# Kernel tuning notes

Hardware: AMD Instinct MI355X
Metric: run time of the kernel (lower is better)

The kernel has to match this reference:

```python
import jax, jax.numpy as jnp
import numpy as np

H = 4  # attention heads
NEG = -1e9

def _ln(x, g, b):
    m = jnp.mean(x, -1, keepdims=True)
    v = jnp.var(x, -1, keepdims=True)
    return g * (x - m) * jax.lax.rsqrt(v + 1e-5) + b

def setup_inputs() -> dict:
    key = jax.random.key(0)
    ks = jax.random.split(key, 32)
    N, E, G, T = 4096, 128, 10, 10
    f32 = jnp.float32
    def w(k, shape, fan):
        return (jax.random.normal(k, shape, f32) / np.sqrt(fan)).astype(f32)
    inp = {
        'lora_states': jax.random.normal(ks[0], (N, 256), f32),
        'temperaments': jax.random.uniform(ks[1], (N, T), f32),
        'adjacency': jax.random.randint(ks[2], (N, N), 0, 2, jnp.int32),
        'memory_bank': jax.random.normal(ks[3], (G, E), f32) * 0.1,
        # lora_state_encoder: Linear(256,512) -> LN -> ReLU -> Linear(512,E) -> LN
        'enc_W1': w(ks[4], (256, 512), 256), 'enc_b1': jnp.zeros((512,), f32),
        'enc_g1': jnp.ones((512,), f32), 'enc_be1': jnp.zeros((512,), f32),
        'enc_W2': w(ks[5], (512, E), 512), 'enc_b2': jnp.zeros((E,), f32),
        'enc_g2': jnp.ones((E,), f32), 'enc_be2': jnp.zeros((E,), f32),
        # TemperamentEncoder: Linear(10,E) + tanh
        'temp_W': w(ks[6], (T, E), T), 'temp_b': jnp.zeros((E,), f32),
        # SocialAttentionLayer (adjacency-masked MHA)
        'Wq': w(ks[7], (E, E), E), 'Wk': w(ks[8], (E, E), E),
        'Wv': w(ks[9], (E, E), E), 'Wo': w(ks[10], (E, E), E),
        # PersonalityModulatedAttention scalar gate over [my_temp; ctx_j]
        'gate_wa': w(ks[11], (E,), E), 'gate_wb': w(ks[12], (E,), E),
        'gate_b': jnp.zeros((), f32),
        # lora_state_decoder: Linear(E,512) -> LN -> ReLU -> Linear(512,256)
        'dec_W1': w(ks[13], (E, 512), E), 'dec_b1': jnp.zeros((512,), f32),
        'dec_g1': jnp.ones((512,), f32), 'dec_be1': jnp.zeros((512,), f32),
        'dec_W2': w(ks[14], (512, 256), 512), 'dec_b2': jnp.zeros((256,), f32),
    }
    return inp

def reference(lora_states, temperaments, adjacency, memory_bank,
              enc_W1, enc_b1, enc_g1, enc_be1, enc_W2, enc_b2, enc_g2, enc_be2,
              temp_W, temp_b, Wq, Wk, Wv, Wo, gate_wa, gate_wb, gate_b,
              dec_W1, dec_b1, dec_g1, dec_be1, dec_W2, dec_b2):
    N = lora_states.shape[0]
    E = Wq.shape[0]
    dh = E // H
    # --- encode LoRA states ---
    h = jax.nn.relu(_ln(lora_states @ enc_W1 + enc_b1, enc_g1, enc_be1))
    emb = _ln(h @ enc_W2 + enc_b2, enc_g2, enc_be2)                  # [N,E]
    # --- temperament embeddings ---
    temp_emb = jnp.tanh(temperaments @ temp_W + temp_b)              # [N,E]
    # --- adjacency-masked multi-head social attention ---
    q = (emb @ Wq).reshape(N, H, dh).transpose(1, 0, 2)              # [H,N,dh]
    k = (emb @ Wk).reshape(N, H, dh).transpose(1, 0, 2)
    v = (emb @ Wv).reshape(N, H, dh).transpose(1, 0, 2)
    scores = jnp.einsum('hnd,hmd->hnm', q, k) / np.sqrt(dh)          # [H,N,N]
    adj = adjacency > 0
    eye = jnp.eye(N, dtype=bool)
    attn = jax.nn.softmax(jnp.where((adj | eye)[None], scores, NEG), axis=-1)
    ctx = jnp.einsum('hnm,hmd->hnd', attn, v).transpose(1, 0, 2).reshape(N, E) @ Wo  # [N,E]
    # --- personality-gated neighbor aggregation (scalar gate per (i,j)) ---
    ti = temp_emb @ gate_wa                                          # [N]
    cj = ctx @ gate_wb                                               # [N]
    gate = jax.nn.sigmoid(ti[:, None] + cj[None, :] + gate_b)        # [N,N]
    nmask = (adj & ~eye).astype(emb.dtype)                           # exclude self
    cnt = nmask.sum(-1)                                              # [N]
    combined = (nmask * gate) @ ctx / jnp.maximum(cnt, 1.0)[:, None] # mean of gated neighbor infos
    updated = emb + 0.2 * jnp.where(cnt[:, None] > 0, combined, 0.0)
    # --- generational memory retrieval: 0.9*emb + 0.1*ancestral ---
    mscore = updated @ memory_bank.T / np.sqrt(E)                    # [N,G]
    ancestral = jax.nn.softmax(mscore, axis=-1) @ memory_bank        # [N,E]
    updated = 0.9 * updated + 0.1 * ancestral
    # --- decode back to LoRA state vectors ---
    d = jax.nn.relu(_ln(updated @ dec_W1 + dec_b1, dec_g1, dec_be1))
    return d @ dec_W2 + dec_b2                                       # [N,256]
```

## Files before the change

### kernel.cpp

```cpp
#include <hip/hip_runtime.h>
#include <math.h>

#define N 4096
#define NHEAD 4
#define SPLIT_ATT 8
#define SPLIT_G 8

__global__ __launch_bounds__(512) void k_enc1(const float* __restrict__ X,
    const float* __restrict__ W, const float* __restrict__ b,
    const float* __restrict__ g, const float* __restrict__ be,
    float* __restrict__ out) {
  __shared__ float xs[8][256];
  __shared__ float hs[8][512];
  const int t = threadIdx.x;
  const int row0 = blockIdx.x * 8;
  {
    const float4* src = reinterpret_cast<const float4*>(X + row0 * 256);
    float4* dst = reinterpret_cast<float4*>(&xs[0][0]);
    dst[t] = src[t];
  }
  __syncthreads();
  float acc[8] = {0.f,0.f,0.f,0.f,0.f,0.f,0.f,0.f};
  for (int k = 0; k < 256; ++k) {
    float w = W[k * 512 + t];
#pragma unroll
    for (int r = 0; r < 8; ++r) acc[r] = fmaf(xs[r][k], w, acc[r]);
  }
  const float bb = b[t];
#pragma unroll
  for (int r = 0; r < 8; ++r) hs[r][t] = acc[r] + bb;
  __syncthreads();
  const int wv = t >> 6, lane = t & 63;
  float v0[8];
  float s1 = 0.f, s2 = 0.f;
#pragma unroll
  for (int kk = 0; kk < 8; ++kk) {
    float x = hs[wv][lane + 64 * kk];
    v0[kk] = x; s1 += x; s2 += x * x;
  }
#pragma unroll
  for (int off = 1; off < 64; off <<= 1) { s1 += __shfl_xor(s1, off); s2 += __shfl_xor(s2, off); }
  const float mean = s1 * (1.f / 512.f);
  const float var = s2 * (1.f / 512.f) - mean * mean;
  const float rstd = rsqrtf(var + 1e-5f);
#pragma unroll
  for (int kk = 0; kk < 8; ++kk) {
    int c = lane + 64 * kk;
    float y = g[c] * (v0[kk] - mean) * rstd + be[c];
    out[(row0 + wv) * 512 + c] = fmaxf(y, 0.f);
  }
}

__global__ __launch_bounds__(128) void k_enc2(const float* __restrict__ X,
    const float* __restrict__ W, const float* __restrict__ b,
    const float* __restrict__ g, const float* __restrict__ be,
    float* __restrict__ out) {
  __shared__ float xs[8][512];
  __shared__ float hs[8][128];
  const int t = threadIdx.x;
  const int row0 = blockIdx.x * 8;
  {
    const float4* src = reinterpret_cast<const float4*>(X + row0 * 512);
    float4* dst = reinterpret_cast<float4*>(&xs[0][0]);
    for (int idx = t; idx < 1024; idx += 128) dst[idx] = src[idx];
  }
  __syncthreads();
  float acc[8] = {0.f,0.f,0.f,0.f,0.f,0.f,0.f,0.f};
  for (int k = 0; k < 512; ++k) {
    float w = W[k * 128 + t];
#pragma unroll
    for (int r = 0; r < 8; ++r) acc[r] = fmaf(xs[r][k], w, acc[r]);
  }
  const float bb = b[t];
#pragma unroll
  for (int r = 0; r < 8; ++r) hs[r][t] = acc[r] + bb;
  __syncthreads();
  const int wv = t >> 6, lane = t & 63;
  for (int rr = 0; rr < 4; ++rr) {
    int row = wv * 4 + rr;
    float a0 = hs[row][lane], a1 = hs[row][lane + 64];
    float s1 = a0 + a1, s2 = a0 * a0 + a1 * a1;
#pragma unroll
    for (int off = 1; off < 64; off <<= 1) { s1 += __shfl_xor(s1, off); s2 += __shfl_xor(s2, off); }
    float mean = s1 * (1.f / 128.f);
    float rstd = rsqrtf(s2 * (1.f / 128.f) - mean * mean + 1e-5f);
    out[(row0 + row) * 128 + lane]      = g[lane] * (a0 - mean) * rstd + be[lane];
    out[(row0 + row) * 128 + lane + 64] = g[lane + 64] * (a1 - mean) * rstd + be[lane + 64];
  }
}

__global__ __launch_bounds__(128) void k_qkv(const float* __restrict__ emb,
    const float* __restrict__ Wq, const float* __restrict__ Wk, const float* __restrict__ Wv,
    float* __restrict__ q, float* __restrict__ k, float* __restrict__ v) {
  __shared__ float xs[8][128];
  const int t = threadIdx.x;
  const int row0 = blockIdx.x * 8;
  {
    const float4* src = reinterpret_cast<const float4*>(emb + row0 * 128);
    float4* dst = reinterpret_cast<float4*>(&xs[0][0]);
    for (int idx = t; idx < 256; idx += 128) dst[idx] = src[idx];
  }
  __syncthreads();
  float aq[8] = {0.f,0.f,0.f,0.f,0.f,0.f,0.f,0.f};
  float ak[8] = {0.f,0.f,0.f,0.f,0.f,0.f,0.f,0.f};
  float av[8] = {0.f,0.f,0.f,0.f,0.f,0.f,0.f,0.f};
  for (int kk = 0; kk < 128; ++kk) {
    float wq = Wq[kk * 128 + t], wk = Wk[kk * 128 + t], wv = Wv[kk * 128 + t];
#pragma unroll
    for (int r = 0; r < 8; ++r) {
      float x = xs[r][kk];
      aq[r] = fmaf(x, wq, aq[r]);
      ak[r] = fmaf(x, wk, ak[r]);
      av[r] = fmaf(x, wv, av[r]);
    }
  }
#pragma unroll
  for (int r = 0; r < 8; ++r) {
    q[(row0 + r) * 128 + t] = aq[r];
    k[(row0 + r) * 128 + t] = ak[r];
    v[(row0 + r) * 128 + t] = av[r];
  }
}

__global__ __launch_bounds__(256) void k_ti(const float* __restrict__ temps,
    const float* __restrict__ tW, const float* __restrict__ tb,
    const float* __restrict__ wa, float* __restrict__ ti_out) {
  __shared__ float tws[1280];
  __shared__ float tbs[128], was[128];
  const int t = threadIdx.x;
  for (int idx = t; idx < 1280; idx += 256) tws[idx] = tW[idx];
  if (t < 128) { tbs[t] = tb[t]; was[t] = wa[t]; }
  __syncthreads();
  const int qi = t & 3;
  const int li = t >> 2;
  const int i = blockIdx.x * 64 + li;
  float tp[10];
#pragma unroll
  for (int c = 0; c < 10; ++c) tp[c] = temps[i * 10 + c];
  float acc = 0.f;
  const int e0 = qi * 32;
  for (int e = e0; e < e0 + 32; ++e) {
    float s = tbs[e];
#pragma unroll
    for (int c = 0; c < 10; ++c) s = fmaf(tp[c], tws[c * 128 + e], s);
    float th = 1.f - 2.f * __fdividef(1.f, __expf(2.f * s) + 1.f);
    acc = fmaf(th, was[e], acc);
  }
  acc += __shfl_xor(acc, 1);
  acc += __shfl_xor(acc, 2);
  if (qi == 0) ti_out[i] = acc;
}

__global__ __launch_bounds__(256, 2) void k_attn(const float* __restrict__ q,
    const float* __restrict__ kk, const float* __restrict__ vv,
    const int* __restrict__ adj, float* __restrict__ pacc, float* __restrict__ pml) {
  __shared__ float Kt[32][128];
  __shared__ float Vt[32][128];
  __shared__ float Mt[64][33];
  const int t = threadIdx.x;
  const int itile = blockIdx.x / SPLIT_ATT;
  const int split = blockIdx.x % SPLIT_ATT;
  const int h = t >> 6;
  const int row = t & 63;
  const int i = itile * 64 + row;
  const int dbase = h * 32;
  float4 q4[8];
  {
    const float4* qp = reinterpret_cast<const float4*>(q + (size_t)i * 128 + dbase);
#pragma unroll
    for (int u = 0; u < 8; ++u) q4[u] = qp[u];
  }
  float m = -1e30f, l = 0.f;
  float4 a[8];
#pragma unroll
  for (int u = 0; u < 8; ++u) a[u] = make_float4(0.f, 0.f, 0.f, 0.f);
  const int j0beg = split * (N / SPLIT_ATT);
  const int j0end = j0beg + (N / SPLIT_ATT);
  for (int j0 = j0beg; j0 < j0end; j0 += 32) {
    __syncthreads();
    {
      const float4* ks = reinterpret_cast<const float4*>(kk + (size_t)j0 * 128);
      const float4* vs = reinterpret_cast<const float4*>(vv + (size_t)j0 * 128);
      float4* kd = reinterpret_cast<float4*>(&Kt[0][0]);
      float4* vd = reinterpret_cast<float4*>(&Vt[0][0]);
#pragma unroll
      for (int u = 0; u < 4; ++u) { kd[t + 256 * u] = ks[t + 256 * u]; vd[t + 256 * u] = vs[t + 256 * u]; }
    }
    {
      const int rr = t >> 2;
      const int c8 = (t & 3) * 8;
      const int gi = itile * 64 + rr;
      const int base = j0 + c8;
      const int4 a4 = *reinterpret_cast<const int4*>(adj + (size_t)gi * N + base);
      const int4 b4 = *reinterpret_cast<const int4*>(adj + (size_t)gi * N + base + 4);
      Mt[rr][c8 + 0] = (a4.x != 0 || gi == base + 0) ? 0.f : -1e9f;
      Mt[rr][c8 + 1] = (a4.y != 0 || gi == base + 1) ? 0.f : -1e9f;
      Mt[rr][c8 + 2] = (a4.z != 0 || gi == base + 2) ? 0.f : -1e9f;
      Mt[rr][c8 + 3] = (a4.w != 0 || gi == base + 3) ? 0.f : -1e9f;
      Mt[rr][c8 + 4] = (b4.x != 0 || gi == base + 4) ? 0.f : -1e9f;
      Mt[rr][c8 + 5] = (b4.y != 0 || gi == base + 5) ? 0.f : -1e9f;
      Mt[rr][c8 + 6] = (b4.z != 0 || gi == base + 6) ? 0.f : -1e9f;
      Mt[rr][c8 + 7] = (b4.w != 0 || gi == base + 7) ? 0.f : -1e9f;
    }
    __syncthreads();
    const float* mrow = Mt[row];
    for (int jj = 0; jj < 32; ++jj) {
      float4 kf[8];
      {
        const float4* kp = reinterpret_cast<const float4*>(&Kt[jj][dbase]);
#pragma unroll
        for (int u = 0; u < 8; ++u) kf[u] = kp[u];
      }
      float s0 = 0.f, s1 = 0.f, s2 = 0.f, s3 = 0.f;
#pragma unroll
      for (int u = 0; u < 8; ++u) {
        s0 = fmaf(q4[u].x, kf[u].x, s0);
        s1 = fmaf(q4[u].y, kf[u].y, s1);
        s2 = fmaf(q4[u].z, kf[u].z, s2);
        s3 = fmaf(q4[u].w, kf[u].w, s3);
      }
      float s = fmaf((s0 + s1) + (s2 + s3), 0.17677669529663687f, mrow[jj]);
      float4 vf[8];
      {
        const float4* vp = reinterpret_cast<const float4*>(&Vt[jj][dbase]);
#pragma unroll
        for (int u = 0; u < 8; ++u) vf[u] = vp[u];
      }
      if (s <= m) {
        float p = __expf(s - m);
        l += p;
#pragma unroll
        for (int u = 0; u < 8; ++u) {
          a[u].x = fmaf(p, vf[u].x, a[u].x);
          a[u].y = fmaf(p, vf[u].y, a[u].y);
          a[u].z = fmaf(p, vf[u].z, a[u].z);
          a[u].w = fmaf(p, vf[u].w, a[u].w);
        }
      } else {
        float r = __expf(m - s);
        l = fmaf(l, r, 1.f);
        m = s;
#pragma unroll
        for (int u = 0; u < 8; ++u) {
          a[u].x = fmaf(a[u].x, r, vf[u].x);
          a[u].y = fmaf(a[u].y, r, vf[u].y);
          a[u].z = fmaf(a[u].z, r, vf[u].z);
          a[u].w = fmaf(a[u].w, r, vf[u].w);
        }
      }
    }
  }
  {
    float4* pa4 = reinterpret_cast<float4*>(pacc + ((size_t)split * N + i) * 128 + dbase);
#pragma unroll
    for (int u = 0; u < 8; ++u) pa4[u] = a[u];
  }
  {
    float2* p2 = reinterpret_cast<float2*>(pml + (((size_t)split * N + i) * NHEAD + h) * 2);
    *p2 = make_float2(m, l);
  }
}

__global__ __launch_bounds__(256) void k_attn_comb(const float* __restrict__ pacc,
    const float* __restrict__ pml, float* __restrict__ attnout) {
  const int gid = blockIdx.x * 256 + threadIdx.x;
  const int i = gid >> 7, e = gid & 127, h = e >> 5;
  float ms[SPLIT_ATT], ls[SPLIT_ATT];
  float M = -1e30f;
#pragma unroll
  for (int s = 0; s < SPLIT_ATT; ++s) {
    size_t idx = (((size_t)s * N + i) * NHEAD + h) * 2;
    ms[s] = pml[idx]; ls[s] = pml[idx + 1];
    M = fmaxf(M, ms[s]);
  }
  float L = 0.f, o = 0.f;
#pragma unroll
  for (int s = 0; s < SPLIT_ATT; ++s) {
    float w = expf(ms[s] - M);
    L = fmaf(ls[s], w, L);
    o = fmaf(pacc[((size_t)(s * N + i)) * 128 + e], w, o);
  }
  attnout[gid] = o / L;
}

__global__ __launch_bounds__(128) void k_ctx(const float* __restrict__ att,
    const float* __restrict__ Wo, const float* __restrict__ wb,
    float* __restrict__ ctx, float* __restrict__ cj) {
  __shared__ float xs[8][128];
  __shared__ float hs[8][128];
  const int t = threadIdx.x;
  const int row0 = blockIdx.x * 8;
  {
    const float4* src = reinterpret_cast<const float4*>(att + row0 * 128);
    float4* dst = reinterpret_cast<float4*>(&xs[0][0]);
    for (int idx = t; idx < 256; idx += 128) dst[idx] = src[idx];
  }
  __syncthreads();
  float acc[8] = {0.f,0.f,0.f,0.f,0.f,0.f,0.f,0.f};
  for (int k = 0; k < 128; ++k) {
    float w = Wo[k * 128 + t];
#pragma unroll
    for (int r = 0; r < 8; ++r) acc[r] = fmaf(xs[r][k], w, acc[r]);
  }
  const float wbt = wb[t];
#pragma unroll
  for (int r = 0; r < 8; ++r) {
    ctx[(row0 + r) * 128 + t] = acc[r];
    hs[r][t] = acc[r] * wbt;
  }
  __syncthreads();
  const int wv = t >> 6, lane = t & 63;
  for (int rr = 0; rr < 4; ++rr) {
    int row = wv * 4 + rr;
    float s1 = hs[row][lane] + hs[row][lane + 64];
#pragma unroll
    for (int off = 1; off < 64; off <<= 1) s1 += __shfl_xor(s1, off);
    if (lane == 0) cj[row0 + row] = s1;
  }
}

__global__ __launch_bounds__(256) void k_gate(const float* __restrict__ ctx,
    const float* __restrict__ cj, const float* __restrict__ ti,
    const int* __restrict__ adj, const float* __restrict__ gbp,
    float* __restrict__ pacc, float* __restrict__ pcnt) {
  __shared__ float cs[64][128];
  __shared__ float gtsT[64][65];
  __shared__ float tis[64];
  __shared__ float cntrow[64];
  __shared__ float pcsum[256];
  const int t = threadIdx.x;
  const int itile = blockIdx.x >> 3;
  const int split = blockIdx.x & 7;
  const int ig = t >> 4;
  const int eg = t & 15;
  const int i0 = itile * 64;
  const float gb = gbp[0];
  if (t < 64) { tis[t] = ti[i0 + t]; cntrow[t] = 0.f; }
  float acc[4][8];
#pragma unroll
  for (int r = 0; r < 4; ++r)
#pragma unroll
    for (int c = 0; c < 8; ++c) acc[r][c] = 0.f;
  const int j0beg = split * (N / SPLIT_G);
  const int j0end = j0beg + (N / SPLIT_G);
  for (int j0 = j0beg; j0 < j0end; j0 += 64) {
    __syncthreads();
    {
      const float4* src = reinterpret_cast<const float4*>(ctx + (size_t)j0 * 128);
      float4* dst = reinterpret_cast<float4*>(&cs[0][0]);
#pragma unroll
      for (int u = 0; u < 8; ++u) dst[t + 256 * u] = src[t + 256 * u];
    }
    {
      const int ii = t >> 2;
      const int jb = (t & 3) * 16;
      const int gi = i0 + ii;
      const float tii = tis[ii];
      const int gjb = j0 + jb;
      float cnt_loc = 0.f;
#pragma unroll
      for (int u = 0; u < 4; ++u) {
        const int4 a4 = *reinterpret_cast<const int4*>(adj + (size_t)gi * N + gjb + u * 4);
        const float4 c4 = *reinterpret_cast<const float4*>(cj + gjb + u * 4);
        const int   aa[4] = {a4.x, a4.y, a4.z, a4.w};
        const float cc[4] = {c4.x, c4.y, c4.z, c4.w};
#pragma unroll
        for (int w = 0; w < 4; ++w) {
          const int jj = jb + u * 4 + w;
          const bool live = (aa[w] != 0) && (gjb + u * 4 + w != gi);
          float gval = 0.f;
          if (live) {
            gval = __fdividef(1.f, 1.f + __expf(-(tii + cc[w] + gb)));
            cnt_loc += 1.f;
          }
          gtsT[jj][ii] = gval;
        }
      }
      pcsum[t] = cnt_loc;
    }
    __syncthreads();
    if (t < 64) {
      cntrow[t] += pcsum[t * 4] + pcsum[t * 4 + 1] + pcsum[t * 4 + 2] + pcsum[t * 4 + 3];
    }
    const int ib = ig * 4;
    const int eb = eg * 8;
    for (int jj = 0; jj < 64; ++jj) {
      const float a0 = gtsT[jj][ib + 0];
      const float a1 = gtsT[jj][ib + 1];
      const float a2 = gtsT[jj][ib + 2];
      const float a3 = gtsT[jj][ib + 3];
      const float4 b0 = *reinterpret_cast<const float4*>(&cs[jj][eb]);
      const float4 b1 = *reinterpret_cast<const float4*>(&cs[jj][eb + 4]);
      const float bv[8] = {b0.x, b0.y, b0.z, b0.w, b1.x, b1.y, b1.z, b1.w};
#pragma unroll
      for (int c = 0; c < 8; ++c) {
        acc[0][c] = fmaf(a0, bv[c], acc[0][c]);
        acc[1][c] = fmaf(a1, bv[c], acc[1][c]);
        acc[2][c] = fmaf(a2, bv[c], acc[2][c]);
        acc[3][c] = fmaf(a3, bv[c], acc[3][c]);
      }
    }
  }
#pragma unroll
  for (int r = 0; r < 4; ++r) {
    float* pa = pacc + ((size_t)split * N + i0 + ig * 4 + r) * 128 + eg * 8;
    float4 o0; o0.x = acc[r][0]; o0.y = acc[r][1]; o0.z = acc[r][2]; o0.w = acc[r][3];
    float4 o1; o1.x = acc[r][4]; o1.y = acc[r][5]; o1.z = acc[r][6]; o1.w = acc[r][7];
    reinterpret_cast<float4*>(pa)[0] = o0;
    reinterpret_cast<float4*>(pa)[1] = o1;
  }
  if (t < 64) pcnt[(size_t)split * N + i0 + t] = cntrow[t];
}

__global__ __launch_bounds__(256) void k_gcomb(const float* __restrict__ GA,
    const float* __restrict__ GC, const float* __restrict__ emb,
    const float* __restrict__ mb, float* __restrict__ upd) {
  __shared__ float mbs[10][128];
  __shared__ float us[2][128];
  const int t = threadIdx.x;
  for (int idx = t; idx < 1280; idx += 256) mbs[idx / 128][idx & 127] = mb[idx];
  const int rs = t >> 7, e = t & 127;
  const int i = blockIdx.x * 2 + rs;
  float a = 0.f;
#pragma unroll
  for (int s = 0; s < SPLIT_G; ++s) a += GA[((size_t)(s * N + i)) * 128 + e];
  float c = 0.f;
#pragma unroll
  for (int s = 0; s < SPLIT_G; ++s) c += GC[s * N + i];
  float comb = a / fmaxf(c, 1.f);
  float u = emb[(size_t)i * 128 + e] + 0.2f * ((c > 0.f) ? comb : 0.f);
  us[rs][e] = u;
  __syncthreads();
  const int wv = t >> 6, lane = t & 63;
  if (wv < 2) {
    const int i2 = blockIdx.x * 2 + wv;
    float u0 = us[wv][lane], u1 = us[wv][lane + 64];
    float sc[10];
#pragma unroll
    for (int g = 0; g < 10; ++g) {
      float p = u0 * mbs[g][lane] + u1 * mbs[g][lane + 64];
#pragma unroll
      for (int off = 1; off < 64; off <<= 1) p += __shfl_xor(p, off);
      sc[g] = p * 0.08838834764831845f;
    }
    float mx = sc[0];
#pragma unroll
    for (int g = 1; g < 10; ++g) mx = fmaxf(mx, sc[g]);
    float sum = 0.f;
#pragma unroll
    for (int g = 0; g < 10; ++g) { sc[g] = expf(sc[g] - mx); sum += sc[g]; }
    float inv = 1.f / sum;
    float anc0 = 0.f, anc1 = 0.f;
#pragma unroll
    for (int g = 0; g < 10; ++g) {
      float pg = sc[g] * inv;
      anc0 = fmaf(pg, mbs[g][lane], anc0);
      anc1 = fmaf(pg, mbs[g][lane + 64], anc1);
    }
    upd[(size_t)i2 * 128 + lane]      = 0.9f * u0 + 0.1f * anc0;
    upd[(size_t)i2 * 128 + lane + 64] = 0.9f * u1 + 0.1f * anc1;
  }
}

__global__ __launch_bounds__(512) void k_dec1(const float* __restrict__ X,
    const float* __restrict__ W, const float* __restrict__ b,
    const float* __restrict__ g, const float* __restrict__ be,
    float* __restrict__ out) {
  __shared__ float xs[8][128];
  __shared__ float hs[8][512];
  const int t = threadIdx.x;
  const int row0 = blockIdx.x * 8;
  if (t < 256) {
    const float4* src = reinterpret_cast<const float4*>(X + row0 * 128);
    float4* dst = reinterpret_cast<float4*>(&xs[0][0]);
    dst[t] = src[t];
  }
  __syncthreads();
  float acc[8] = {0.f,0.f,0.f,0.f,0.f,0.f,0.f,0.f};
  for (int k = 0; k < 128; ++k) {
    float w = W[k * 512 + t];
#pragma unroll
    for (int r = 0; r < 8; ++r) acc[r] = fmaf(xs[r][k], w, acc[r]);
  }
  const float bb = b[t];
#pragma unroll
  for (int r = 0; r < 8; ++r) hs[r][t] = acc[r] + bb;
  __syncthreads();
  const int wv = t >> 6, lane = t & 63;
  float v0[8];
  float s1 = 0.f, s2 = 0.f;
#pragma unroll
  for (int kk = 0; kk < 8; ++kk) {
    float x = hs[wv][lane + 64 * kk];
    v0[kk] = x; s1 += x; s2 += x * x;
  }
#pragma unroll
  for (int off = 1; off < 64; off <<= 1) { s1 += __shfl_xor(s1, off); s2 += __shfl_xor(s2, off); }
  const float mean = s1 * (1.f / 512.f);
  const float var = s2 * (1.f / 512.f) - mean * mean;
  const float rstd = rsqrtf(var + 1e-5f);
#pragma unroll
  for (int kk = 0; kk < 8; ++kk) {
    int c = lane + 64 * kk;
    float y = g[c] * (v0[kk] - mean) * rstd + be[c];
    out[(row0 + wv) * 512 + c] = fmaxf(y, 0.f);
  }
}

__global__ __launch_bounds__(256) void k_dec2(const float* __restrict__ X,
    const float* __restrict__ W, const float* __restrict__ b, float* __restrict__ out) {
  __shared__ float xs[8][512];
  const int t = threadIdx.x;
  const int row0 = blockIdx.x * 8;
  {
    const float4* src = reinterpret_cast<const float4*>(X + row0 * 512);
    float4* dst = reinterpret_cast<float4*>(&xs[0][0]);
    for (int idx = t; idx < 1024; idx += 256) dst[idx] = src[idx];
  }
  __syncthreads();
  float acc[8] = {0.f,0.f,0.f,0.f,0.f,0.f,0.f,0.f};
  for (int k = 0; k < 512; ++k) {
    float w = W[k * 256 + t];
#pragma unroll
    for (int r = 0; r < 8; ++r) acc[r] = fmaf(xs[r][k], w, acc[r]);
  }
  const float bb = b[t];
#pragma unroll
  for (int r = 0; r < 8; ++r) out[(row0 + r) * 256 + t] = acc[r] + bb;
}

extern "C" void kernel_launch(void* const* d_in, const int* in_sizes, int n_in,
                              void* d_out, int out_size, void* d_ws, size_t ws_size,
                              hipStream_t stream) {
  const float* lora   = (const float*)d_in[0];
  const float* temps  = (const float*)d_in[1];
  const int*   adj    = (const int*)d_in[2];
  const float* mb     = (const float*)d_in[3];
  const float* enc_W1 = (const float*)d_in[4];
  const float* enc_b1 = (const float*)d_in[5];
  const float* enc_g1 = (const float*)d_in[6];
  const float* enc_be1= (const float*)d_in[7];
  const float* enc_W2 = (const float*)d_in[8];
  const float* enc_b2 = (const float*)d_in[9];
  const float* enc_g2 = (const float*)d_in[10];
  const float* enc_be2= (const float*)d_in[11];
  const float* temp_W = (const float*)d_in[12];
  const float* temp_b = (const float*)d_in[13];
  const float* Wq     = (const float*)d_in[14];
  const float* Wk     = (const float*)d_in[15];
  const float* Wv     = (const float*)d_in[16];
  const float* Wo     = (const float*)d_in[17];
  const float* g_wa   = (const float*)d_in[18];
  const float* g_wb   = (const float*)d_in[19];
  const float* g_b    = (const float*)d_in[20];
  const float* dec_W1 = (const float*)d_in[21];
  const float* dec_b1 = (const float*)d_in[22];
  const float* dec_g1 = (const float*)d_in[23];
  const float* dec_be1= (const float*)d_in[24];
  const float* dec_W2 = (const float*)d_in[25];
  const float* dec_b2 = (const float*)d_in[26];

  float* ws = (float*)d_ws;
  float* H1  = ws;
  float* EMB = H1 + (size_t)N * 512;
  float* Q   = EMB + (size_t)N * 128;
  float* K   = Q + (size_t)N * 128;
  float* V   = K + (size_t)N * 128;
  float* ATT = V + (size_t)N * 128;
  float* CTX = ATT + (size_t)N * 128;
  float* TI  = CTX + (size_t)N * 128;
  float* CJ  = TI + N;
  float* PA  = CJ + N;
  float* PML = PA + (size_t)8 * N * 128;
  float* UPD = ATT;
  float* GA  = PA;
  float* GC  = PML;
  float* DEC = H1;

  k_enc1<<<N / 8, 512, 0, stream>>>(lora, enc_W1, enc_b1, enc_g1, enc_be1, H1);
  k_enc2<<<N / 8, 128, 0, stream>>>(H1, enc_W2, enc_b2, enc_g2, enc_be2, EMB);
  k_ti<<<N / 64, 256, 0, stream>>>(temps, temp_W, temp_b, g_wa, TI);
  k_qkv<<<N / 8, 128, 0, stream>>>(EMB, Wq, Wk, Wv, Q, K, V);
  k_attn<<<(N / 64) * SPLIT_ATT, 256, 0, stream>>>(Q, K, V, adj, PA, PML);
  k_attn_comb<<<(N * 128) / 256, 256, 0, stream>>>(PA, PML, ATT);
  k_ctx<<<N / 8, 128, 0, stream>>>(ATT, Wo, g_wb, CTX, CJ);
  k_gate<<<(N / 64) * SPLIT_G, 256, 0, stream>>>(CTX, CJ, TI, adj, g_b, GA, GC);
  k_gcomb<<<N / 2, 256, 0, stream>>>(GA, GC, EMB, mb, UPD);
  k_dec1<<<N / 8, 512, 0, stream>>>(UPD, dec_W1, dec_b1, dec_g1, dec_be1, DEC);
  k_dec2<<<N / 8, 256, 0, stream>>>(DEC, dec_W2, dec_b2, (float*)d_out);
}
```

Baseline: 615.5 us.

## Pack adjacency into bitmask once and reuse in attention and gate kernels

Adds a kernel that ballots the int32 adjacency matrix into a 1-bit-per-entry mask, which the attention and gate kernels then read instead of the full int32 matrix. The adjacency is read once from memory rather than twice, and the later reads shrink by 32x. The attention inner loop is also restructured to process 8 keys at a time with a single running-max rescale per group, using a larger 64-key K/V tile and no shared mask tile. The QKV projection switches to 512-thread blocks covering 16 rows. The cost is an extra launch and one full pass over the adjacency, plus higher shared memory use in the attention kernel.

```diff
diff --git a/kernel.cpp b/kernel.cpp
--- a/kernel.cpp
+++ b/kernel.cpp
@@ -5,6 +5,21 @@
 #define NHEAD 4
 #define SPLIT_ATT 8
 #define SPLIT_G 8
+
+__global__ __launch_bounds__(256) void k_bm(const int* __restrict__ adj,
+    unsigned int* __restrict__ bmw) {
+  const int lane = threadIdx.x & 63;
+  const int wid = threadIdx.x >> 6;
+  const long total = (long)N * N / 64;
+  long g = (long)blockIdx.x * 4 + wid;
+  const long stride = (long)gridDim.x * 4;
+  for (; g < total; g += stride) {
+    int e = adj[g * 64 + lane];
+    unsigned long long mask = __ballot(e != 0);
+    if (lane == 0)  bmw[g * 2]     = (unsigned int)(mask & 0xFFFFFFFFull);
+    if (lane == 32) bmw[g * 2 + 1] = (unsigned int)(mask >> 32);
+  }
+}
 
 __global__ __launch_bounds__(512) void k_enc1(const float* __restrict__ X,
     const float* __restrict__ W, const float* __restrict__ b,
@@ -89,36 +104,39 @@
   }
 }
 
-__global__ __launch_bounds__(128) void k_qkv(const float* __restrict__ emb,
+__global__ __launch_bounds__(512) void k_qkv(const float* __restrict__ emb,
     const float* __restrict__ Wq, const float* __restrict__ Wk, const float* __restrict__ Wv,
     float* __restrict__ q, float* __restrict__ k, float* __restrict__ v) {
-  __shared__ float xs[8][128];
-  const int t = threadIdx.x;
-  const int row0 = blockIdx.x * 8;
+  __shared__ float xs[16][128];
+  const int t = threadIdx.x;
+  const int col = t & 127;
+  const int grp = t >> 7;
+  const int row0 = blockIdx.x * 16;
   {
     const float4* src = reinterpret_cast<const float4*>(emb + row0 * 128);
     float4* dst = reinterpret_cast<float4*>(&xs[0][0]);
-    for (int idx = t; idx < 256; idx += 128) dst[idx] = src[idx];
-  }
-  __syncthreads();
-  float aq[8] = {0.f,0.f,0.f,0.f,0.f,0.f,0.f,0.f};
-  float ak[8] = {0.f,0.f,0.f,0.f,0.f,0.f,0.f,0.f};
-  float av[8] = {0.f,0.f,0.f,0.f,0.f,0.f,0.f,0.f};
+    dst[t] = src[t];
+  }
+  __syncthreads();
+  float aq[4] = {0.f,0.f,0.f,0.f};
+  float ak[4] = {0.f,0.f,0.f,0.f};
+  float av[4] = {0.f,0.f,0.f,0.f};
   for (int kk = 0; kk < 128; ++kk) {
-    float wq = Wq[kk * 128 + t], wk = Wk[kk * 128 + t], wv = Wv[kk * 128 + t];
-#pragma unroll
-    for (int r = 0; r < 8; ++r) {
-      float x = xs[r][kk];
+    float wq = Wq[kk * 128 + col], wk = Wk[kk * 128 + col], wv = Wv[kk * 128 + col];
+#pragma unroll
+    for (int r = 0; r < 4; ++r) {
+      float x = xs[grp * 4 + r][kk];
       aq[r] = fmaf(x, wq, aq[r]);
       ak[r] = fmaf(x, wk, ak[r]);
       av[r] = fmaf(x, wv, av[r]);
     }
   }
 #pragma unroll
-  for (int r = 0; r < 8; ++r) {
-    q[(row0 + r) * 128 + t] = aq[r];
-    k[(row0 + r) * 128 + t] = ak[r];
-    v[(row0 + r) * 128 + t] = av[r];
+  for (int r = 0; r < 4; ++r) {
+    const int row = row0 + grp * 4 + r;
+    q[row * 128 + col] = aq[r];
+    k[row * 128 + col] = ak[r];
+    v[row * 128 + col] = av[r];
   }
 }
 
@@ -153,10 +171,10 @@
 
 __global__ __launch_bounds__(256, 2) void k_attn(const float* __restrict__ q,
     const float* __restrict__ kk, const float* __restrict__ vv,
-    const int* __restrict__ adj, float* __restrict__ pacc, float* __restrict__ pml) {
-  __shared__ float Kt[32][128];
-  __shared__ float Vt[32][128];
-  __shared__ float Mt[64][33];
+    const unsigned int* __restrict__ bmw,
+    float* __restrict__ pacc, float* __restrict__ pml) {
+  __shared__ float Kt[64][128];
+  __shared__ float Vt[64][128];
   const int t = threadIdx.x;
   const int itile = blockIdx.x / SPLIT_ATT;
   const int split = blockIdx.x % SPLIT_ATT;
@@ -176,7 +194,7 @@
   for (int u = 0; u < 8; ++u) a[u] = make_float4(0.f, 0.f, 0.f, 0.f);
   const int j0beg = split * (N / SPLIT_ATT);
   const int j0end = j0beg + (N / SPLIT_ATT);
-  for (int j0 = j0beg; j0 < j0end; j0 += 32) {
+  for (int j0 = j0beg; j0 < j0end; j0 += 64) {
     __syncthreads();
     {
       const float4* ks = reinterpret_cast<const float4*>(kk + (size_t)j0 * 128);
@@ -184,68 +202,55 @@
       float4* kd = reinterpret_cast<float4*>(&Kt[0][0]);
       float4* vd = reinterpret_cast<float4*>(&Vt[0][0]);
 #pragma unroll
-      for (int u = 0; u < 4; ++u) { kd[t + 256 * u] = ks[t + 256 * u]; vd[t + 256 * u] = vs[t + 256 * u]; }
-    }
-    {
-      const int rr = t >> 2;
-      const int c8 = (t & 3) * 8;
-      const int gi = itile * 64 + rr;
-      const int base = j0 + c8;
-      const int4 a4 = *reinterpret_cast<const int4*>(adj + (size_t)gi * N + base);
-      const int4 b4 = *reinterpret_cast<const int4*>(adj + (size_t)gi * N + base + 4);
-      Mt[rr][c8 + 0] = (a4.x != 0 || gi == base + 0) ? 0.f : -1e9f;
-      Mt[rr][c8 + 1] = (a4.y != 0 || gi == base + 1) ? 0.f : -1e9f;
-      Mt[rr][c8 + 2] = (a4.z != 0 || gi == base + 2) ? 0.f : -1e9f;
-      Mt[rr][c8 + 3] = (a4.w != 0 || gi == base + 3) ? 0.f : -1e9f;
-      Mt[rr][c8 + 4] = (b4.x != 0 || gi == base + 4) ? 0.f : -1e9f;
-      Mt[rr][c8 + 5] = (b4.y != 0 || gi == base + 5) ? 0.f : -1e9f;
-      Mt[rr][c8 + 6] = (b4.z != 0 || gi == base + 6) ? 0.f : -1e9f;
-      Mt[rr][c8 + 7] = (b4.w != 0 || gi == base + 7) ? 0.f : -1e9f;
-    }
+      for (int u = 0; u < 8; ++u) { kd[t + 256 * u] = ks[t + 256 * u]; vd[t + 256 * u] = vs[t + 256 * u]; }
+    }
+    const uint2 mw = *reinterpret_cast<const uint2*>(bmw + (size_t)i * 128 + (j0 >> 5));
+    const int eyeoff = i - j0;
     __syncthreads();
-    const float* mrow = Mt[row];
-    for (int jj = 0; jj < 32; ++jj) {
-      float4 kf[8];
-      {
-        const float4* kp = reinterpret_cast<const float4*>(&Kt[jj][dbase]);
-#pragma unroll
-        for (int u = 0; u < 8; ++u) kf[u] = kp[u];
+    for (int sub = 0; sub < 8; ++sub) {
+      const int jb = sub * 8;
+      unsigned mbits = ((sub < 4 ? mw.x : mw.y) >> ((sub & 3) * 8)) & 0xFFu;
+      if (((unsigned)(eyeoff - jb)) < 8u) mbits |= (1u << (eyeoff - jb));
+      float sarr[8];
+#pragma unroll
+      for (int u = 0; u < 8; ++u) {
+        const float4* kp = reinterpret_cast<const float4*>(&Kt[jb + u][dbase]);
+        float4 kf[8];
+#pragma unroll
+        for (int w = 0; w < 8; ++w) kf[w] = kp[w];
+        float s0 = 0.f, s1 = 0.f, s2 = 0.f, s3 = 0.f;
+#pragma unroll
+        for (int w = 0; w < 8; ++w) {
+          s0 = fmaf(q4[w].x, kf[w].x, s0);
+          s1 = fmaf(q4[w].y, kf[w].y, s1);
+          s2 = fmaf(q4[w].z, kf[w].z, s2);
+          s3 = fmaf(q4[w].w, kf[w].w, s3);
+        }
+        sarr[u] = fmaf((s0 + s1) + (s2 + s3), 0.17677669529663687f,
+                       ((mbits >> u) & 1u) ? 0.f : -1e9f);
       }
-      float s0 = 0.f, s1 = 0.f, s2 = 0.f, s3 = 0.f;
+      float smax = fmaxf(fmaxf(fmaxf(sarr[0], sarr[1]), fmaxf(sarr[2], sarr[3])),
+                         fmaxf(fmaxf(sarr[4], sarr[5]), fmaxf(sarr[6], sarr[7])));
+      float mnew = fmaxf(m, smax);
+      float r = __expf(m - mnew);
+      m = mnew;
+      l *= r;
 #pragma unroll
       for (int u = 0; u < 8; ++u) {
-        s0 = fmaf(q4[u].x, kf[u].x, s0);
-        s1 = fmaf(q4[u].y, kf[u].y, s1);
-        s2 = fmaf(q4[u].z, kf[u].z, s2);
-        s3 = fmaf(q4[u].w, kf[u].w, s3);
+        a[u].x *= r; a[u].y *= r; a[u].z *= r; a[u].w *= r;
       }
-      float s = fmaf((s0 + s1) + (s2 + s3), 0.17677669529663687f, mrow[jj]);
-      float4 vf[8];
-      {
-        const float4* vp = reinterpret_cast<const float4*>(&Vt[jj][dbase]);
-#pragma unroll
-        for (int u = 0; u < 8; ++u) vf[u] = vp[u];
-      }
-      if (s <= m) {
-        float p = __expf(s - m);
+#pragma unroll
+      for (int u = 0; u < 8; ++u) {
+        float p = __expf(sarr[u] - m);
         l += p;
-#pragma unroll
-        for (int u = 0; u < 8; ++u) {
-          a[u].x = fmaf(p, vf[u].x, a[u].x);
-          a[u].y = fmaf(p, vf[u].y, a[u].y);
-          a[u].z = fmaf(p, vf[u].z, a[u].z);
-          a[u].w = fmaf(p, vf[u].w, a[u].w);
-        }
-      } else {
-        float r = __expf(m - s);
-        l = fmaf(l, r, 1.f);
-        m = s;
-#pragma unroll
-        for (int u = 0; u < 8; ++u) {
-          a[u].x = fmaf(a[u].x, r, vf[u].x);
-          a[u].y = fmaf(a[u].y, r, vf[u].y);
-          a[u].z = fmaf(a[u].z, r, vf[u].z);
-          a[u].w = fmaf(a[u].w, r, vf[u].w);
+        const float4* vp = reinterpret_cast<const float4*>(&Vt[jb + u][dbase]);
+#pragma unroll
+        for (int w = 0; w < 8; ++w) {
+          float4 vf = vp[w];
+          a[w].x = fmaf(p, vf.x, a[w].x);
+          a[w].y = fmaf(p, vf.y, a[w].y);
+          a[w].z = fmaf(p, vf.z, a[w].z);
+          a[w].w = fmaf(p, vf.w, a[w].w);
         }
       }
     }
@@ -321,7 +326,7 @@
 
 __global__ __launch_bounds__(256) void k_gate(const float* __restrict__ ctx,
     const float* __restrict__ cj, const float* __restrict__ ti,
-    const int* __restrict__ adj, const float* __restrict__ gbp,
+    const unsigned int* __restrict__ bmw, const float* __restrict__ gbp,
     float* __restrict__ pacc, float* __restrict__ pcnt) {
   __shared__ float cs[64][128];
   __shared__ float gtsT[64][65];
@@ -353,28 +358,29 @@
     }
     {
       const int ii = t >> 2;
-      const int jb = (t & 3) * 16;
+      const int qd = t & 3;
+      const int jb = qd * 16;
       const int gi = i0 + ii;
       const float tii = tis[ii];
-      const int gjb = j0 + jb;
+      const unsigned word = bmw[(size_t)gi * 128 + (j0 >> 5) + (qd >> 1)];
+      const unsigned mb16 = (word >> ((qd & 1) * 16)) & 0xFFFFu;
       float cnt_loc = 0.f;
-#pragma unroll
-      for (int u = 0; u < 4; ++u) {
-        const int4 a4 = *reinterpret_cast<const int4*>(adj + (size_t)gi * N + gjb + u * 4);
-        const float4 c4 = *reinterpret_cast<const float4*>(cj + gjb + u * 4);
-        const int   aa[4] = {a4.x, a4.y, a4.z, a4.w};
-        const float cc[4] = {c4.x, c4.y, c4.z, c4.w};
-#pragma unroll
-        for (int w = 0; w < 4; ++w) {
-          const int jj = jb + u * 4 + w;
-          const bool live = (aa[w] != 0) && (gjb + u * 4 + w != gi);
-          float gval = 0.f;
-          if (live) {
-            gval = __fdividef(1.f, 1.f + __expf(-(tii + cc[w] + gb)));
-            cnt_loc += 1.f;
-          }
-          gtsT[jj][ii] = gval;
+      const float4* cjp = reinterpret_cast<const float4*>(cj + j0 + jb);
+      float4 cv[4];
+#pragma unroll
+      for (int u = 0; u < 4; ++u) cv[u] = cjp[u];
+      const float cva[16] = {cv[0].x,cv[0].y,cv[0].z,cv[0].w, cv[1].x,cv[1].y,cv[1].z,cv[1].w,
+                             cv[2].x,cv[2].y,cv[2].z,cv[2].w, cv[3].x,cv[3].y,cv[3].z,cv[3].w};
+#pragma unroll
+      for (int w = 0; w < 16; ++w) {
+        const int gj = j0 + jb + w;
+        const bool live = ((mb16 >> w) & 1u) && (gj != gi);
+        float gval = 0.f;
+        if (live) {
+          gval = __fdividef(1.f, 1.f + __expf(-(tii + cva[w] + gb)));
+          cnt_loc += 1.f;
         }
+        gtsT[jb + w][ii] = gval;
       }
       pcsum[t] = cnt_loc;
     }
@@ -572,19 +578,21 @@
   float* CJ  = TI + N;
   float* PA  = CJ + N;
   float* PML = PA + (size_t)8 * N * 128;
+  unsigned int* BMW = (unsigned int*)(PML + (size_t)8 * N * NHEAD * 2);
   float* UPD = ATT;
   float* GA  = PA;
   float* GC  = PML;
   float* DEC = H1;
 
+  k_bm<<<512, 256, 0, stream>>>(adj, BMW);
   k_enc1<<<N / 8, 512, 0, stream>>>(lora, enc_W1, enc_b1, enc_g1, enc_be1, H1);
   k_enc2<<<N / 8, 128, 0, stream>>>(H1, enc_W2, enc_b2, enc_g2, enc_be2, EMB);
   k_ti<<<N / 64, 256, 0, stream>>>(temps, temp_W, temp_b, g_wa, TI);
-  k_qkv<<<N / 8, 128, 0, stream>>>(EMB, Wq, Wk, Wv, Q, K, V);
-  k_attn<<<(N / 64) * SPLIT_ATT, 256, 0, stream>>>(Q, K, V, adj, PA, PML);
+  k_qkv<<<N / 16, 512, 0, stream>>>(EMB, Wq, Wk, Wv, Q, K, V);
+  k_attn<<<(N / 64) * SPLIT_ATT, 256, 0, stream>>>(Q, K, V, BMW, PA, PML);
   k_attn_comb<<<(N * 128) / 256, 256, 0, stream>>>(PA, PML, ATT);
   k_ctx<<<N / 8, 128, 0, stream>>>(ATT, Wo, g_wb, CTX, CJ);
-  k_gate<<<(N / 64) * SPLIT_G, 256, 0, stream>>>(CTX, CJ, TI, adj, g_b, GA, GC);
+  k_gate<<<(N / 64) * SPLIT_G, 256, 0, stream>>>(CTX, CJ, TI, BMW, g_b, GA, GC);
   k_gcomb<<<N / 2, 256, 0, stream>>>(GA, GC, EMB, mb, UPD);
   k_dec1<<<N / 8, 512, 0, stream>>>(UPD, dec_W1, dec_b1, dec_g1, dec_be1, DEC);
   k_dec2<<<N / 8, 256, 0, stream>>>(DEC, dec_W2, dec_b2, (float*)d_out);
```

Result: slower. 716.7 us (+16.4%).
